# Kernel optimization log

Hardware: AMD Instinct MI355X
Metric: run time of the kernel (lower is better)

## Reference

```python
import jax, jax.numpy as jnp
import numpy as np

B, N, D = 8, 1024, 768
H = 12
HD = D // H  # 64
SCALE = HD ** (-0.5)


def setup_inputs() -> dict:
    key = jax.random.key(0)
    ks = jax.random.split(key, 11)
    s = 0.02
    return {
        "x": jax.random.normal(ks[0], (B, N, D), dtype=jnp.float32),
        "w_q": jax.random.normal(ks[1], (D, D), dtype=jnp.float32) * s,
        "b_q": jax.random.normal(ks[2], (D,), dtype=jnp.float32) * s,
        "w_k": jax.random.normal(ks[3], (D, D), dtype=jnp.float32) * s,
        "b_k": jax.random.normal(ks[4], (D,), dtype=jnp.float32) * s,
        "w_v": jax.random.normal(ks[5], (D, D), dtype=jnp.float32) * s,
        "b_v": jax.random.normal(ks[6], (D,), dtype=jnp.float32) * s,
        "w_qt": jax.random.normal(ks[7], (D, D), dtype=jnp.float32) * s,
        "b_qt": jax.random.normal(ks[8], (D,), dtype=jnp.float32) * s,
        "w_p": jax.random.normal(ks[9], (D, D), dtype=jnp.float32) * s,
        "b_p": jax.random.normal(ks[10], (D,), dtype=jnp.float32) * s,
    }


def _heads(y):
    # [B,N,D] -> [B,H,N,HD]
    b, n, d = y.shape
    return y.reshape(b, n, H, HD).transpose(0, 2, 1, 3)


def reference(x, w_q, b_q, w_k, b_k, w_v, b_v, w_qt, b_qt, w_p, b_p):
    # torch nn.Linear: y = x @ W.T + b
    q = _heads(x @ w_q.T + b_q)
    k = _heads(x @ w_k.T + b_k)
    v = _heads(x @ w_v.T + b_v)
    q_tilde = _heads(x @ w_qt.T + b_qt)
    # NOTE: source divides by self.scale = head_dim**-0.5 (i.e. multiplies by sqrt(hd)); reproduced faithfully
    corr = jnp.einsum("bhnd,bhmd->bhnm", q_tilde, k) / SCALE
    scores = jnp.einsum("bhnd,bhmd->bhnm", q, k) / SCALE + corr
    attn = jax.nn.softmax(scores, axis=-1)
    out = jnp.einsum("bhnm,bhmd->bhnd", attn, v)  # [B,H,N,HD]
    out = out.transpose(0, 2, 1, 3).reshape(x.shape[0], x.shape[1], D)
    out = out @ w_p.T + b_p
    return out, corr
```

## Files before the change

kernel.cpp:

```cpp
#include <hip/hip_runtime.h>

typedef __bf16 bf16_t;
typedef __bf16 bf16x8 __attribute__((ext_vector_type(8)));
typedef __bf16 bf16x4 __attribute__((ext_vector_type(4)));
typedef float f32x4 __attribute__((ext_vector_type(4)));

constexpr int BATCH = 8;
constexpr int NSEQ = 1024;
constexpr int DMODEL = 768;
constexpr int NH = 12;
constexpr int HDIM = 64;
constexpr int MROWS = BATCH * NSEQ;
constexpr int WSZ = DMODEL * DMODEL;
constexpr float L2E = 1.44269504088896f;

#define AS1(p) ((const __attribute__((address_space(1))) void*)(p))
#define AS3(p) ((__attribute__((address_space(3))) void*)(p))

__global__ __launch_bounds__(256) void prep_w(
    const float* __restrict__ wq, const float* __restrict__ wqt,
    const float* __restrict__ wk, const float* __restrict__ wv,
    const float* __restrict__ wp, const float* __restrict__ bq,
    const float* __restrict__ bqt, ushort* __restrict__ wb_,
    float* __restrict__ bqs, float* __restrict__ bqt8)
{
    int i = blockIdx.x * 256 + threadIdx.x;
    bf16_t* w = (bf16_t*)wb_;
    float a = wq[i], b = wqt[i];
    w[i]            = (bf16_t)(8.0f * (a + b));
    w[WSZ + i]      = (bf16_t)(8.0f * b);
    w[2*WSZ + i]    = (bf16_t)wk[i];
    w[3*WSZ + i]    = (bf16_t)wv[i];
    w[4*WSZ + i]    = (bf16_t)wp[i];
    if (i < DMODEL) {
        bqs[i]  = 8.0f * (bq[i] + bqt[i]);
        bqt8[i] = 8.0f * bqt[i];
    }
}

__global__ __launch_bounds__(256) void conv_x(const float* __restrict__ x,
                                              ushort* __restrict__ xb_)
{
    int i = (blockIdx.x * 256 + threadIdx.x) * 4;
    float4 v = *(const float4*)(x + i);
    bf16x4 r = { (bf16_t)v.x, (bf16_t)v.y, (bf16_t)v.z, (bf16_t)v.w };
    *(bf16x4*)((bf16_t*)xb_ + i) = r;
}

__device__ __forceinline__ void gemm_core(
    const bf16_t* __restrict__ A, const bf16_t* __restrict__ W,
    bf16_t* As, bf16_t* Bs, int m0, int n0, int tid, f32x4 acc[4][4])
{
    const int lane = tid & 63, wave = tid >> 6;
    const int g = lane >> 4, c = lane & 15;
    const int wm = wave >> 1, wn = wave & 1;

    const int r_b = tid >> 3;
    const int koff = 8 * ((tid & 7) ^ (r_b & 7));
    const size_t arow = (size_t)(m0 + r_b) * DMODEL + koff;
    const size_t brow = (size_t)(n0 + r_b) * DMODEL + koff;
    char* As_base = (char*)As + (tid & ~63) * 16;
    char* Bs_base = (char*)Bs + (tid & ~63) * 16;

    for (int k0 = 0; k0 < DMODEL; k0 += 64) {
        __syncthreads();
#pragma unroll
        for (int i = 0; i < 4; i++)
            __builtin_amdgcn_global_load_lds(
                AS1(A + arow + k0 + (size_t)i * 32 * DMODEL),
                AS3(As_base + i * 4096), 16, 0, 0);
#pragma unroll
        for (int i = 0; i < 4; i++)
            __builtin_amdgcn_global_load_lds(
                AS1(W + brow + k0 + (size_t)i * 32 * DMODEL),
                AS3(Bs_base + i * 4096), 16, 0, 0);
        __syncthreads();
#pragma unroll
        for (int kk = 0; kk < 2; kk++) {
            bf16x8 af[4], bfr[4];
#pragma unroll
            for (int mt = 0; mt < 4; mt++) {
                int r = wm * 64 + mt * 16 + c;
                af[mt] = *(const bf16x8*)(As + r * 64 + ((kk * 4 + g) ^ (r & 7)) * 8);
            }
#pragma unroll
            for (int nt = 0; nt < 4; nt++) {
                int r = wn * 64 + nt * 16 + c;
                bfr[nt] = *(const bf16x8*)(Bs + r * 64 + ((kk * 4 + g) ^ (r & 7)) * 8);
            }
#pragma unroll
            for (int mt = 0; mt < 4; mt++)
#pragma unroll
                for (int nt = 0; nt < 4; nt++)
                    acc[mt][nt] = __builtin_amdgcn_mfma_f32_16x16x32_bf16(
                        af[mt], bfr[nt], acc[mt][nt], 0, 0, 0);
        }
    }
}

__global__ __launch_bounds__(256) void gemm_qkv(
    const ushort* __restrict__ xb_, const ushort* __restrict__ wb_,
    const float* __restrict__ bqs, const float* __restrict__ bqt8,
    const float* __restrict__ bk, const float* __restrict__ bv,
    ushort* __restrict__ o0, ushort* __restrict__ o1,
    ushort* __restrict__ o2, ushort* __restrict__ o3)
{
    __shared__ alignas(16) bf16_t As[128 * 64];
    __shared__ alignas(16) bf16_t Bs[128 * 64];
    const int bid = blockIdx.x;
    const int gid = (bid & 7) * 192 + (bid >> 3);
    const int z = gid / 384;
    const int rr = gid % 384;
    const int m0 = (rr / 6) * 128, n0 = (rr % 6) * 128;

    const bf16_t* A = (const bf16_t*)xb_;
    const bf16_t* W = (const bf16_t*)wb_ + (size_t)z * WSZ;
    const float* bias = (z == 0) ? bqs : (z == 1) ? bqt8 : (z == 2) ? bk : bv;
    bf16_t* outp = (bf16_t*)((z == 0) ? o0 : (z == 1) ? o1 : (z == 2) ? o2 : o3);
    f32x4 acc[4][4] = {};
    gemm_core(A, W, As, Bs, m0, n0, threadIdx.x, acc);

    const int tid = threadIdx.x, lane = tid & 63, wave = tid >> 6;
    const int g = lane >> 4, c = lane & 15;
    const int wm = wave >> 1, wn = wave & 1;
#pragma unroll
    for (int mt = 0; mt < 4; mt++)
#pragma unroll
        for (int nt = 0; nt < 4; nt++) {
            int col = n0 + wn * 64 + nt * 16 + c;
            int h = col >> 6, hd = col & 63;
            float bsv = bias[col];
            if (z == 3) {
                int row0 = m0 + wm * 64 + mt * 16 + 4 * g;
                int b = row0 >> 10, ns0 = row0 & 1023;
                bf16x4 pb = { (bf16_t)(acc[mt][nt][0] + bsv),
                              (bf16_t)(acc[mt][nt][1] + bsv),
                              (bf16_t)(acc[mt][nt][2] + bsv),
                              (bf16_t)(acc[mt][nt][3] + bsv) };
                *(bf16x4*)(outp + ((size_t)(b * NH + h) * HDIM + hd) * NSEQ + ns0) = pb;
            } else {
#pragma unroll
                for (int j = 0; j < 4; j++) {
                    int row = m0 + wm * 64 + mt * 16 + 4 * g + j;
                    int b = row >> 10, ns = row & 1023;
                    outp[(((size_t)b * NH + h) * NSEQ + ns) * HDIM + hd] =
                        (bf16_t)(acc[mt][nt][j] + bsv);
                }
            }
        }
}

__global__ __launch_bounds__(256) void gemm_out(
    const ushort* __restrict__ ao_, const ushort* __restrict__ wp_,
    const float* __restrict__ bp, float* __restrict__ out)
{
    __shared__ alignas(16) bf16_t As[128 * 64];
    __shared__ alignas(16) bf16_t Bs[128 * 64];
    const int bid = blockIdx.x;
    const int gid = (bid & 7) * 48 + (bid >> 3);
    const int m0 = (gid / 6) * 128, n0 = (gid % 6) * 128;

    const bf16_t* A = (const bf16_t*)ao_;
    const bf16_t* W = (const bf16_t*)wp_;
    f32x4 acc[4][4] = {};
    gemm_core(A, W, As, Bs, m0, n0, threadIdx.x, acc);

    const int tid = threadIdx.x, lane = tid & 63, wave = tid >> 6;
    const int g = lane >> 4, c = lane & 15;
    const int wm = wave >> 1, wn = wave & 1;
#pragma unroll
    for (int mt = 0; mt < 4; mt++)
#pragma unroll
        for (int nt = 0; nt < 4; nt++) {
            int col = n0 + wn * 64 + nt * 16 + c;
            float bsv = bp[col];
#pragma unroll
            for (int j = 0; j < 4; j++) {
                int row = m0 + wm * 64 + mt * 16 + 4 * g + j;
                out[(size_t)row * DMODEL + col] = acc[mt][nt][j] + bsv;
            }
        }
}

__global__ __launch_bounds__(256, 2) void attn_kernel(
    const ushort* __restrict__ qs_, const ushort* __restrict__ qt_,
    const ushort* __restrict__ kb_, const ushort* __restrict__ vt_,
    ushort* __restrict__ ao_, float* __restrict__ corr)
{
    __shared__ alignas(16) bf16_t VT[2][64 * 64];
    __shared__ alignas(16) bf16_t P[4][32 * 72];
    const bf16_t* QS = (const bf16_t*)qs_;
    const bf16_t* QT = (const bf16_t*)qt_;
    const bf16_t* Kb = (const bf16_t*)kb_;
    const bf16_t* Vt = (const bf16_t*)vt_;
    bf16_t* Ob = (bf16_t*)ao_;

    const int tid = threadIdx.x;
    const int w = tid >> 6, lane = tid & 63;
    const int g = lane >> 4, c = lane & 15;
    const int bid = blockIdx.x;
    const int gid = (bid & 7) * 96 + (bid >> 3);
    const int bh = gid >> 3, qb = gid & 7;
    const int q00 = qb * 128 + w * 32;
    const size_t base = (size_t)bh * (NSEQ * HDIM);

    bf16x8 qsf[2][2], qtf[2][2];
#pragma unroll
    for (int s = 0; s < 2; s++)
#pragma unroll
        for (int kk = 0; kk < 2; kk++) {
            const size_t qrow = base + (size_t)(q00 + s * 16 + c) * HDIM + kk * 32 + 8 * g;
            qsf[s][kk] = *(const bf16x8*)(QS + qrow);
            qtf[s][kk] = *(const bf16x8*)(QT + qrow);
        }
    f32x4 oacc[2][4] = {};
    float mrun[2], lrun[2];
#pragma unroll
    for (int s = 0; s < 2; s++) { mrun[s] = -3e30f; lrun[s] = 0.f; }

    float* corr_b = corr + (size_t)bh * (NSEQ * NSEQ);

    const int hd0_ = tid >> 3, ch0_ = tid & 7;
    const int hd1_ = hd0_ + 32;
    const int vtoff0 = hd0_ * 64 + (ch0_ ^ (hd0_ & 7)) * 8;
    const int vtoff1 = hd1_ * 64 + (ch0_ ^ (hd1_ & 7)) * 8;

    bf16x8 vrA = *(const bf16x8*)(Vt + base + (size_t)hd0_ * NSEQ + ch0_ * 8);
    bf16x8 vrB = *(const bf16x8*)(Vt + base + (size_t)hd1_ * NSEQ + ch0_ * 8);
    bf16x8 kf[4][2];
#pragma unroll
    for (int kvt = 0; kvt < 4; kvt++) {
        const size_t krow = base + (size_t)(kvt * 16 + c) * HDIM + 8 * g;
        kf[kvt][0] = *(const bf16x8*)(Kb + krow);
        kf[kvt][1] = *(const bf16x8*)(Kb + krow + 32);
    }
    *(bf16x8*)(VT[0] + vtoff0) = vrA;
    *(bf16x8*)(VT[0] + vtoff1) = vrB;
    asm volatile("s_waitcnt lgkmcnt(0)" ::: "memory");
    __builtin_amdgcn_sched_barrier(0);
    __builtin_amdgcn_s_barrier();

    for (int t = 0; t < 16; t++) {
        const int kv0 = t * 64;
        const int kvn = kv0 + 64;
        bf16_t* vtc = VT[t & 1];
        bf16_t* vtn = VT[(t + 1) & 1];
        if (t < 15) {
            vrA = *(const bf16x8*)(Vt + base + (size_t)hd0_ * NSEQ + kvn + ch0_ * 8);
            vrB = *(const bf16x8*)(Vt + base + (size_t)hd1_ * NSEQ + kvn + ch0_ * 8);
        }
        __builtin_amdgcn_s_setprio(1);
        f32x4 sv[2][4];
#pragma unroll
        for (int kvt = 0; kvt < 4; kvt++) {
#pragma unroll
            for (int s = 0; s < 2; s++) {
                f32x4 sa = {0.f, 0.f, 0.f, 0.f};
                f32x4 ca = {0.f, 0.f, 0.f, 0.f};
                sa = __builtin_amdgcn_mfma_f32_16x16x32_bf16(kf[kvt][0], qsf[s][0], sa, 0, 0, 0);
                sa = __builtin_amdgcn_mfma_f32_16x16x32_bf16(kf[kvt][1], qsf[s][1], sa, 0, 0, 0);
                ca = __builtin_amdgcn_mfma_f32_16x16x32_bf16(kf[kvt][0], qtf[s][0], ca, 0, 0, 0);
                ca = __builtin_amdgcn_mfma_f32_16x16x32_bf16(kf[kvt][1], qtf[s][1], ca, 0, 0, 0);
                sv[s][kvt] = sa;
                *(f32x4*)(corr_b + (size_t)(q00 + s * 16 + c) * NSEQ + kv0 + kvt * 16 + 4 * g) = ca;
            }
        }
        __builtin_amdgcn_s_setprio(0);
#pragma unroll
        for (int s = 0; s < 2; s++) {
            f32x4 mm;
#pragma unroll
            for (int j = 0; j < 4; j++)
                mm[j] = fmaxf(fmaxf(sv[s][0][j], sv[s][1][j]),
                              fmaxf(sv[s][2][j], sv[s][3][j]));
            float tm = fmaxf(fmaxf(mm[0], mm[1]), fmaxf(mm[2], mm[3]));
            tm = fmaxf(tm, __shfl_xor(tm, 16));
            tm = fmaxf(tm, __shfl_xor(tm, 32));
            if (__any(tm > mrun[s] + 8.0f)) {
                float newm = fmaxf(mrun[s], tm);
                float scl = exp2f((mrun[s] - newm) * L2E);
                mrun[s] = newm;
                lrun[s] *= scl;
#pragma unroll
                for (int j = 0; j < 4; j++) {
                    float scj = __shfl(scl, 4 * g + j);
#pragma unroll
                    for (int nt = 0; nt < 4; nt++) oacc[s][nt][j] *= scj;
                }
            }
            const float mneg = mrun[s] * L2E;
            float ps = 0.f;
#pragma unroll
            for (int kvt = 0; kvt < 4; kvt++)
#pragma unroll
                for (int j = 0; j < 4; j++) {
                    float p = exp2f(__builtin_fmaf(sv[s][kvt][j], L2E, -mneg));
                    sv[s][kvt][j] = p;
                    ps += p;
                }
            ps += __shfl_xor(ps, 16);
            ps += __shfl_xor(ps, 32);
            lrun[s] += ps;
#pragma unroll
            for (int kvt = 0; kvt < 4; kvt++) {
                bf16x4 pb = { (bf16_t)sv[s][kvt][0], (bf16_t)sv[s][kvt][1],
                              (bf16_t)sv[s][kvt][2], (bf16_t)sv[s][kvt][3] };
                *(bf16x4*)(&P[w][(s * 16 + c) * 72 + kvt * 16 + 4 * g]) = pb;
            }
        }
        if (t < 15) {
#pragma unroll
            for (int kvt = 0; kvt < 4; kvt++) {
                const size_t krow = base + (size_t)(kvn + kvt * 16 + c) * HDIM + 8 * g;
                kf[kvt][0] = *(const bf16x8*)(Kb + krow);
                kf[kvt][1] = *(const bf16x8*)(Kb + krow + 32);
            }
        }
        __builtin_amdgcn_s_setprio(1);
#pragma unroll
        for (int kk = 0; kk < 2; kk++) {
#pragma unroll
            for (int nt = 0; nt < 4; nt++) {
                const int hd = nt * 16 + c;
                bf16x8 vf = *(const bf16x8*)(&vtc[hd * 64 + (((kk * 4 + g) ^ (hd & 7)) * 8)]);
#pragma unroll
                for (int s = 0; s < 2; s++) {
                    bf16x8 pa = *(const bf16x8*)(&P[w][(s * 16 + c) * 72 + kk * 32 + 8 * g]);
                    oacc[s][nt] = __builtin_amdgcn_mfma_f32_16x16x32_bf16(pa, vf, oacc[s][nt], 0, 0, 0);
                }
            }
        }
        __builtin_amdgcn_s_setprio(0);
        if (t < 15) {
            *(bf16x8*)(vtn + vtoff0) = vrA;
            *(bf16x8*)(vtn + vtoff1) = vrB;
        }
        asm volatile("s_waitcnt lgkmcnt(0)" ::: "memory");
        __builtin_amdgcn_sched_barrier(0);
        __builtin_amdgcn_s_barrier();
    }
    const int b = bh / NH, h = bh % NH;
#pragma unroll
    for (int s = 0; s < 2; s++) {
        float lj[4];
#pragma unroll
        for (int j = 0; j < 4; j++) lj[j] = __shfl(lrun[s], 4 * g + j);
#pragma unroll
        for (int nt = 0; nt < 4; nt++)
#pragma unroll
            for (int j = 0; j < 4; j++) {
                float val = oacc[s][nt][j] / lj[j];
                Ob[(size_t)(b * NSEQ + q00 + s * 16 + 4 * g + j) * DMODEL + h * HDIM + nt * 16 + c] =
                    (bf16_t)val;
            }
    }
}

extern "C" void kernel_launch(void* const* d_in, const int* in_sizes, int n_in,
                              void* d_out, int out_size, void* d_ws, size_t ws_size,
                              hipStream_t stream)
{
    const float* x   = (const float*)d_in[0];
    const float* wq  = (const float*)d_in[1];
    const float* bq  = (const float*)d_in[2];
    const float* wk  = (const float*)d_in[3];
    const float* bk  = (const float*)d_in[4];
    const float* wv  = (const float*)d_in[5];
    const float* bv  = (const float*)d_in[6];
    const float* wqt = (const float*)d_in[7];
    const float* bqt = (const float*)d_in[8];
    const float* wp  = (const float*)d_in[9];
    const float* bp  = (const float*)d_in[10];

    char* ws = (char*)d_ws;
    ushort* xb   = (ushort*)(ws);
    ushort* wb   = (ushort*)(ws + 12582912);
    float*  bqs  = (float*)(ws + 18481152);
    float*  bqt8 = (float*)(ws + 18485248);
    ushort* qs   = (ushort*)(ws + 18489344);
    ushort* qt   = qs + 6291456;
    ushort* kb   = qt + 6291456;
    ushort* vt   = kb + 6291456;
    ushort* ao   = vt + 6291456;

    float* out  = (float*)d_out;
    float* corr = out + (size_t)6291456;

    prep_w<<<2304, 256, 0, stream>>>(wq, wqt, wk, wv, wp, bq, bqt, wb, bqs, bqt8);
    conv_x<<<6144, 256, 0, stream>>>(x, xb);
    gemm_qkv<<<1536, 256, 0, stream>>>(xb, wb, bqs, bqt8, bk, bv, qs, qt, kb, vt);
    attn_kernel<<<768, 256, 0, stream>>>(qs, qt, kb, vt, ao, corr);
    gemm_out<<<384, 256, 0, stream>>>(ao, wb + (size_t)4 * WSZ, bp, out);
}
```

Measured before the change: 227.1 us.

## Halve attention query tile per wave to double grid and occupancy

Each wave of the attention kernel now handles 16 query rows instead of 32, so a block covers 64 queries and the grid grows from 768 to 1536 blocks. Register and LDS use per block drop, and launch bounds ask for 4 blocks per CU so more waves can hide latency. The cost is that every K/V tile is loaded from global memory and staged in LDS twice as often per query, and the block barrier is amortised over less MFMA work.

```diff
diff --git a/kernel.cpp b/kernel.cpp
--- a/kernel.cpp
+++ b/kernel.cpp
@@ -182,13 +182,13 @@
         }
 }
 
-__global__ __launch_bounds__(256, 2) void attn_kernel(
+__global__ __launch_bounds__(256, 4) void attn_kernel(
     const ushort* __restrict__ qs_, const ushort* __restrict__ qt_,
     const ushort* __restrict__ kb_, const ushort* __restrict__ vt_,
     ushort* __restrict__ ao_, float* __restrict__ corr)
 {
     __shared__ alignas(16) bf16_t VT[2][64 * 64];
-    __shared__ alignas(16) bf16_t P[4][32 * 72];
+    __shared__ alignas(16) bf16_t P[4][16 * 72];
     const bf16_t* QS = (const bf16_t*)qs_;
     const bf16_t* QT = (const bf16_t*)qt_;
     const bf16_t* Kb = (const bf16_t*)kb_;
@@ -199,24 +199,20 @@
     const int w = tid >> 6, lane = tid & 63;
     const int g = lane >> 4, c = lane & 15;
     const int bid = blockIdx.x;
-    const int gid = (bid & 7) * 96 + (bid >> 3);
-    const int bh = gid >> 3, qb = gid & 7;
-    const int q00 = qb * 128 + w * 32;
+    const int gid = (bid & 7) * 192 + (bid >> 3);
+    const int bh = gid >> 4, qb = gid & 15;
+    const int q0 = qb * 64 + w * 16;
     const size_t base = (size_t)bh * (NSEQ * HDIM);
 
-    bf16x8 qsf[2][2], qtf[2][2];
-#pragma unroll
-    for (int s = 0; s < 2; s++)
-#pragma unroll
-        for (int kk = 0; kk < 2; kk++) {
-            const size_t qrow = base + (size_t)(q00 + s * 16 + c) * HDIM + kk * 32 + 8 * g;
-            qsf[s][kk] = *(const bf16x8*)(QS + qrow);
-            qtf[s][kk] = *(const bf16x8*)(QT + qrow);
-        }
-    f32x4 oacc[2][4] = {};
-    float mrun[2], lrun[2];
-#pragma unroll
-    for (int s = 0; s < 2; s++) { mrun[s] = -3e30f; lrun[s] = 0.f; }
+    bf16x8 qsf[2], qtf[2];
+#pragma unroll
+    for (int kk = 0; kk < 2; kk++) {
+        const size_t qrow = base + (size_t)(q0 + c) * HDIM + kk * 32 + 8 * g;
+        qsf[kk] = *(const bf16x8*)(QS + qrow);
+        qtf[kk] = *(const bf16x8*)(QT + qrow);
+    }
+    f32x4 oacc[4] = {};
+    float mrun = -3e30f, lrun = 0.f;
 
     float* corr_b = corr + (size_t)bh * (NSEQ * NSEQ);
 
@@ -250,63 +246,56 @@
             vrB = *(const bf16x8*)(Vt + base + (size_t)hd1_ * NSEQ + kvn + ch0_ * 8);
         }
         __builtin_amdgcn_s_setprio(1);
-        f32x4 sv[2][4];
+        f32x4 sv[4];
 #pragma unroll
         for (int kvt = 0; kvt < 4; kvt++) {
-#pragma unroll
-            for (int s = 0; s < 2; s++) {
-                f32x4 sa = {0.f, 0.f, 0.f, 0.f};
-                f32x4 ca = {0.f, 0.f, 0.f, 0.f};
-                sa = __builtin_amdgcn_mfma_f32_16x16x32_bf16(kf[kvt][0], qsf[s][0], sa, 0, 0, 0);
-                sa = __builtin_amdgcn_mfma_f32_16x16x32_bf16(kf[kvt][1], qsf[s][1], sa, 0, 0, 0);
-                ca = __builtin_amdgcn_mfma_f32_16x16x32_bf16(kf[kvt][0], qtf[s][0], ca, 0, 0, 0);
-                ca = __builtin_amdgcn_mfma_f32_16x16x32_bf16(kf[kvt][1], qtf[s][1], ca, 0, 0, 0);
-                sv[s][kvt] = sa;
-                *(f32x4*)(corr_b + (size_t)(q00 + s * 16 + c) * NSEQ + kv0 + kvt * 16 + 4 * g) = ca;
-            }
+            f32x4 sa = {0.f, 0.f, 0.f, 0.f};
+            f32x4 ca = {0.f, 0.f, 0.f, 0.f};
+            sa = __builtin_amdgcn_mfma_f32_16x16x32_bf16(kf[kvt][0], qsf[0], sa, 0, 0, 0);
+            sa = __builtin_amdgcn_mfma_f32_16x16x32_bf16(kf[kvt][1], qsf[1], sa, 0, 0, 0);
+            ca = __builtin_amdgcn_mfma_f32_16x16x32_bf16(kf[kvt][0], qtf[0], ca, 0, 0, 0);
+            ca = __builtin_amdgcn_mfma_f32_16x16x32_bf16(kf[kvt][1], qtf[1], ca, 0, 0, 0);
+            sv[kvt] = sa;
+            *(f32x4*)(corr_b + (size_t)(q0 + c) * NSEQ + kv0 + kvt * 16 + 4 * g) = ca;
         }
         __builtin_amdgcn_s_setprio(0);
-#pragma unroll
-        for (int s = 0; s < 2; s++) {
-            f32x4 mm;
-#pragma unroll
-            for (int j = 0; j < 4; j++)
-                mm[j] = fmaxf(fmaxf(sv[s][0][j], sv[s][1][j]),
-                              fmaxf(sv[s][2][j], sv[s][3][j]));
-            float tm = fmaxf(fmaxf(mm[0], mm[1]), fmaxf(mm[2], mm[3]));
-            tm = fmaxf(tm, __shfl_xor(tm, 16));
-            tm = fmaxf(tm, __shfl_xor(tm, 32));
-            if (__any(tm > mrun[s] + 8.0f)) {
-                float newm = fmaxf(mrun[s], tm);
-                float scl = exp2f((mrun[s] - newm) * L2E);
-                mrun[s] = newm;
-                lrun[s] *= scl;
-#pragma unroll
-                for (int j = 0; j < 4; j++) {
-                    float scj = __shfl(scl, 4 * g + j);
-#pragma unroll
-                    for (int nt = 0; nt < 4; nt++) oacc[s][nt][j] *= scj;
-                }
-            }
-            const float mneg = mrun[s] * L2E;
-            float ps = 0.f;
-#pragma unroll
-            for (int kvt = 0; kvt < 4; kvt++)
-#pragma unroll
-                for (int j = 0; j < 4; j++) {
-                    float p = exp2f(__builtin_fmaf(sv[s][kvt][j], L2E, -mneg));
-                    sv[s][kvt][j] = p;
-                    ps += p;
-                }
-            ps += __shfl_xor(ps, 16);
-            ps += __shfl_xor(ps, 32);
-            lrun[s] += ps;
-#pragma unroll
-            for (int kvt = 0; kvt < 4; kvt++) {
-                bf16x4 pb = { (bf16_t)sv[s][kvt][0], (bf16_t)sv[s][kvt][1],
-                              (bf16_t)sv[s][kvt][2], (bf16_t)sv[s][kvt][3] };
-                *(bf16x4*)(&P[w][(s * 16 + c) * 72 + kvt * 16 + 4 * g]) = pb;
-            }
+        f32x4 mm;
+#pragma unroll
+        for (int j = 0; j < 4; j++)
+            mm[j] = fmaxf(fmaxf(sv[0][j], sv[1][j]), fmaxf(sv[2][j], sv[3][j]));
+        float tm = fmaxf(fmaxf(mm[0], mm[1]), fmaxf(mm[2], mm[3]));
+        tm = fmaxf(tm, __shfl_xor(tm, 16));
+        tm = fmaxf(tm, __shfl_xor(tm, 32));
+        if (__any(tm > mrun + 8.0f)) {
+            float newm = fmaxf(mrun, tm);
+            float scl = exp2f((mrun - newm) * L2E);
+            mrun = newm;
+            lrun *= scl;
+#pragma unroll
+            for (int j = 0; j < 4; j++) {
+                float scj = __shfl(scl, 4 * g + j);
+#pragma unroll
+                for (int nt = 0; nt < 4; nt++) oacc[nt][j] *= scj;
+            }
+        }
+        const float mneg = mrun * L2E;
+        float ps = 0.f;
+#pragma unroll
+        for (int kvt = 0; kvt < 4; kvt++)
+#pragma unroll
+            for (int j = 0; j < 4; j++) {
+                float p = exp2f(__builtin_fmaf(sv[kvt][j], L2E, -mneg));
+                sv[kvt][j] = p;
+                ps += p;
+            }
+        ps += __shfl_xor(ps, 16);
+        ps += __shfl_xor(ps, 32);
+        lrun += ps;
+#pragma unroll
+        for (int kvt = 0; kvt < 4; kvt++) {
+            bf16x4 pb = { (bf16_t)sv[kvt][0], (bf16_t)sv[kvt][1],
+                          (bf16_t)sv[kvt][2], (bf16_t)sv[kvt][3] };
+            *(bf16x4*)(&P[w][c * 72 + kvt * 16 + 4 * g]) = pb;
         }
         if (t < 15) {
 #pragma unroll
@@ -323,11 +312,8 @@
             for (int nt = 0; nt < 4; nt++) {
                 const int hd = nt * 16 + c;
                 bf16x8 vf = *(const bf16x8*)(&vtc[hd * 64 + (((kk * 4 + g) ^ (hd & 7)) * 8)]);
-#pragma unroll
-                for (int s = 0; s < 2; s++) {
-                    bf16x8 pa = *(const bf16x8*)(&P[w][(s * 16 + c) * 72 + kk * 32 + 8 * g]);
-                    oacc[s][nt] = __builtin_amdgcn_mfma_f32_16x16x32_bf16(pa, vf, oacc[s][nt], 0, 0, 0);
-                }
+                bf16x8 pa = *(const bf16x8*)(&P[w][c * 72 + kk * 32 + 8 * g]);
+                oacc[nt] = __builtin_amdgcn_mfma_f32_16x16x32_bf16(pa, vf, oacc[nt], 0, 0, 0);
             }
         }
         __builtin_amdgcn_s_setprio(0);
@@ -340,20 +326,17 @@
         __builtin_amdgcn_s_barrier();
     }
     const int b = bh / NH, h = bh % NH;
-#pragma unroll
-    for (int s = 0; s < 2; s++) {
-        float lj[4];
-#pragma unroll
-        for (int j = 0; j < 4; j++) lj[j] = __shfl(lrun[s], 4 * g + j);
-#pragma unroll
-        for (int nt = 0; nt < 4; nt++)
-#pragma unroll
-            for (int j = 0; j < 4; j++) {
-                float val = oacc[s][nt][j] / lj[j];
-                Ob[(size_t)(b * NSEQ + q00 + s * 16 + 4 * g + j) * DMODEL + h * HDIM + nt * 16 + c] =
-                    (bf16_t)val;
-            }
-    }
+    float lj[4];
+#pragma unroll
+    for (int j = 0; j < 4; j++) lj[j] = __shfl(lrun, 4 * g + j);
+#pragma unroll
+    for (int nt = 0; nt < 4; nt++)
+#pragma unroll
+        for (int j = 0; j < 4; j++) {
+            float val = oacc[nt][j] / lj[j];
+            Ob[(size_t)(b * NSEQ + q0 + 4 * g + j) * DMODEL + h * HDIM + nt * 16 + c] =
+                (bf16_t)val;
+        }
 }
 
 extern "C" void kernel_launch(void* const* d_in, const int* in_sizes, int n_in,
@@ -389,6 +372,6 @@
     prep_w<<<2304, 256, 0, stream>>>(wq, wqt, wk, wv, wp, bq, bqt, wb, bqs, bqt8);
     conv_x<<<6144, 256, 0, stream>>>(x, xb);
     gemm_qkv<<<1536, 256, 0, stream>>>(xb, wb, bqs, bqt8, bk, bv, qs, qt, kb, vt);
-    attn_kernel<<<768, 256, 0, stream>>>(qs, qt, kb, vt, ao, corr);
+    attn_kernel<<<1536, 256, 0, stream>>>(qs, qt, kb, vt, ao, corr);
     gemm_out<<<384, 256, 0, stream>>>(ao, wb + (size_t)4 * WSZ, bp, out);
 }
```

After: 240.8 us. +6.1%, slower.
